# Kernel optimization log

Hardware: AMD Instinct MI355X
Metric: run time of the kernel (lower is better)

## Reference

```python
import jax, jax.numpy as jnp
import numpy as np

N_ATOMS = 100000
N_BONDS = 250000
MAX_NB = 6
HIDDEN = 256
DEPTH = 3
NUM_MOLS = 2000
ATOM_FDIM = 133
BOND_FDIM = 147


def setup_inputs() -> dict:
    key = jax.random.key(0)
    ks = jax.random.split(key, 12)
    return {
        "f_atoms": jax.random.normal(ks[0], (N_ATOMS, ATOM_FDIM), jnp.float32),
        "f_bonds": jax.random.normal(ks[1], (N_BONDS, BOND_FDIM), jnp.float32),
        "w_atoms": jax.random.uniform(ks[2], (N_ATOMS,), jnp.float32),
        "w_bonds": jax.random.uniform(ks[3], (N_BONDS,), jnp.float32),
        "W_i": jax.random.normal(ks[4], (BOND_FDIM, HIDDEN), jnp.float32) * 0.05,
        "W_h": jax.random.normal(ks[5], (HIDDEN, HIDDEN), jnp.float32) * 0.05,
        "W_o": jax.random.normal(ks[6], (ATOM_FDIM + HIDDEN, HIDDEN), jnp.float32) * 0.05,
        "b_o": jnp.zeros((HIDDEN,), jnp.float32),
        "degree_of_polym": jax.random.uniform(ks[7], (NUM_MOLS,), jnp.float32),
        "a2b": jax.random.randint(ks[8], (N_ATOMS, MAX_NB), 0, N_BONDS, jnp.int32),
        "b2a": jax.random.randint(ks[9], (N_BONDS,), 0, N_ATOMS, jnp.int32),
        "b2revb": jax.random.randint(ks[10], (N_BONDS,), 0, N_BONDS, jnp.int32),
        "mol_ids": jnp.sort(jax.random.randint(ks[11], (N_ATOMS,), 0, NUM_MOLS, jnp.int32)),
    }


def reference(f_atoms, f_bonds, w_atoms, w_bonds, W_i, W_h, W_o, b_o,
              degree_of_polym, a2b, b2a, b2revb, mol_ids):
    # input-layer: bond features -> hidden messages
    inp = f_bonds @ W_i                      # [n_bonds, H]
    message = jax.nn.relu(inp)

    for _ in range(DEPTH - 1):
        # gather incoming bond messages per atom and weight them
        nei_msg = message[a2b]               # [n_atoms, max_nb, H]
        nei_w = w_bonds[a2b]                 # [n_atoms, max_nb]
        a_message = (nei_msg * nei_w[..., None]).sum(axis=1)  # [n_atoms, H]
        # directed message: total at source atom minus reverse bond
        message = a_message[b2a] - message[b2revb]             # [n_bonds, H]
        message = jax.nn.relu(inp + message @ W_h)             # dropout p=0 (eval)

    # final atom-level readout
    nei_msg = message[a2b] * w_bonds[a2b][..., None]
    a_message = nei_msg.sum(axis=1)                            # [n_atoms, H]
    a_input = jnp.concatenate([f_atoms, a_message], axis=1)    # [n_atoms, atom_fdim+H]
    atom_hiddens = jax.nn.relu(a_input @ W_o + b_o)            # [n_atoms, H]

    # per-molecule weighted mean aggregation (a_scope loop -> segment_sum)
    weighted = atom_hiddens * w_atoms[:, None]
    mol_sum = jax.ops.segment_sum(weighted, mol_ids, num_segments=NUM_MOLS)
    w_sum = jax.ops.segment_sum(w_atoms, mol_ids, num_segments=NUM_MOLS)
    safe_w = jnp.where(w_sum > 0, w_sum, 1.0)
    mol_vecs = jnp.where((w_sum > 0)[:, None], mol_sum / safe_w[:, None], 0.0)
    mol_vecs = degree_of_polym[:, None] * mol_vecs             # [num_mols, H]
    return mol_vecs
```

## Files before the change

### kernel.cpp

```cpp
#include <hip/hip_runtime.h>
#include <hip/hip_bf16.h>

typedef unsigned short u16;
typedef __bf16 bf16x8v __attribute__((ext_vector_type(8)));
typedef float f32x4v __attribute__((ext_vector_type(4)));
typedef float f32x4u __attribute__((ext_vector_type(4))) __attribute__((aligned(4)));

__device__ __forceinline__ float bf2f(u16 u) {
    union { float f; unsigned int i; } c; c.i = ((unsigned int)u) << 16; return c.f;
}
__device__ __forceinline__ u16 f2bf(float f) {
    union { float f; unsigned int i; } c; c.f = f;
    unsigned int i = c.i;
    unsigned int lsb = (i >> 16) & 1u;
    i += 0x7fffu + lsb;
    return (u16)(i >> 16);
}
__device__ __forceinline__ float lo16(unsigned u) { return bf2f((u16)(u & 0xffff)); }
__device__ __forceinline__ float hi16(unsigned u) { return bf2f((u16)(u >> 16)); }
__device__ __forceinline__ unsigned pack2(float lo, float hi) {
    return (unsigned)f2bf(lo) | ((unsigned)f2bf(hi) << 16);
}

__device__ __forceinline__ unsigned neg2(unsigned u) { return u ^ 0x80008000u; }
__device__ __forceinline__ unsigned relu_neg2(unsigned u) {
    unsigned s = u & 0x80008000u;
    unsigned m = (s - (s >> 15)) | s;
    return (u ^ 0x80008000u) & ~m;
}

__device__ __forceinline__ bf16x8v load_cvt8(const float* __restrict__ rowp, int k, int kmax) {
    union { unsigned u[4]; bf16x8v v; } r;
#pragma unroll
    for (int g = 0; g < 2; ++g) {
        int kk = k + g * 4;
        float f0, f1, f2, f3;
        if (kk + 3 < kmax) {
            f32x4u q = *(const f32x4u*)(rowp + kk);
            f0 = q.x; f1 = q.y; f2 = q.z; f3 = q.w;
        } else {
            f0 = (kk + 0 < kmax) ? rowp[kk + 0] : 0.f;
            f1 = (kk + 1 < kmax) ? rowp[kk + 1] : 0.f;
            f2 = (kk + 2 < kmax) ? rowp[kk + 2] : 0.f;
            f3 = (kk + 3 < kmax) ? rowp[kk + 3] : 0.f;
        }
        r.u[g * 2]     = pack2(f0, f1);
        r.u[g * 2 + 1] = pack2(f2, f3);
    }
    return r.v;
}

__global__ void pack_w(const float* __restrict__ W, u16* __restrict__ Wt, int K, int Kpad) {
    int idx = blockIdx.x * 256 + threadIdx.x;
    if (idx >= 256 * Kpad) return;
    int n = idx / Kpad, k = idx % Kpad;
    float v = (k < K) ? W[k * 256 + n] : 0.f;
    Wt[idx] = f2bf(v);
}

__global__ void pack_wo(const float* __restrict__ W_o, u16* __restrict__ Wt) {
    int idx = blockIdx.x * 256 + threadIdx.x;
    if (idx >= 256 * 448) return;
    int n = idx / 448, k = idx % 448;
    float v;
    if (k < 256)       v = W_o[(133 + k) * 256 + n];
    else if (k < 389)  v = W_o[(k - 256) * 256 + n];
    else               v = 0.f;
    Wt[idx] = f2bf(v);
}

template <bool RELU>
__global__ __launch_bounds__(256)
void gather16(const u16* __restrict__ msg, const int* __restrict__ a2b,
              const float* __restrict__ w_bonds, u16* __restrict__ out, int nAtoms) {
    int t = threadIdx.x;
    int atom = blockIdx.x * 8 + (t >> 5);
    int co = (t & 31) * 8;
    if (atom >= nAtoms) return;
    float a[8] = {0.f, 0.f, 0.f, 0.f, 0.f, 0.f, 0.f, 0.f};
#pragma unroll
    for (int j = 0; j < 6; ++j) {
        int b = a2b[atom * 6 + j];
        float w = w_bonds[b];
        uint4 v = *(const uint4*)(msg + (size_t)b * 256 + co);
        unsigned p[4] = {v.x, v.y, v.z, v.w};
#pragma unroll
        for (int q = 0; q < 4; ++q) {
            float m0 = lo16(p[q]), m1 = hi16(p[q]);
            if (RELU) { m0 = fmaxf(m0, 0.f); m1 = fmaxf(m1, 0.f); }
            a[q * 2]     += w * m0;
            a[q * 2 + 1] += w * m1;
        }
    }
    uint4 o;
    o.x = pack2(a[0], a[1]); o.y = pack2(a[2], a[3]);
    o.z = pack2(a[4], a[5]); o.w = pack2(a[6], a[7]);
    *(uint4*)(out + (size_t)atom * 256 + co) = o;
}

__global__ __launch_bounds__(512, 2)
void gemm_in(const float* __restrict__ A, const u16* __restrict__ Bt, int M,
             u16* __restrict__ out0) {
    constexpr int KPAD = 160, KMAX = 147, ASTR = 147;
    constexpr int LSTR = KPAD + 8;
    __shared__ u16 Bs[256 * LSTR];
    const int tid = threadIdx.x;
    const int wave = tid >> 6;
    const int lane = tid & 63;
    const int mrow = lane & 15;
    const int quad = lane >> 4;

    constexpr int KC = KPAD / 8;
    for (int i = tid; i < 256 * KC; i += 512) {
        int r = i / KC, kc = i % KC;
        *(uint4*)&Bs[r * LSTR + kc * 8] = *(const uint4*)&Bt[(size_t)r * KPAD + kc * 8];
    }
    __syncthreads();

    for (long chunk = blockIdx.x; chunk * 256 < (long)M; chunk += gridDim.x) {
        const long mbase = chunk * 256 + wave * 32;
        const float* rowp[2];
#pragma unroll
        for (int t = 0; t < 2; ++t) {
            long r = mbase + t * 16 + mrow;
            if (r >= M) r = M - 1;
            rowp[t] = A + r * ASTR;
        }

        f32x4v acc[2][16];
#pragma unroll
        for (int t = 0; t < 2; ++t)
#pragma unroll
            for (int j = 0; j < 16; ++j) acc[t][j] = (f32x4v){0.f, 0.f, 0.f, 0.f};

#pragma unroll 2
        for (int k0 = 0; k0 < KPAD; k0 += 32) {
            bf16x8v a_frag[2];
#pragma unroll
            for (int t = 0; t < 2; ++t)
                a_frag[t] = load_cvt8(rowp[t], k0 + quad * 8, KMAX);
#pragma unroll
            for (int jg = 0; jg < 4; ++jg) {
                bf16x8v b_frag[4];
#pragma unroll
                for (int j4 = 0; j4 < 4; ++j4)
                    b_frag[j4] = *(const bf16x8v*)&Bs[((jg * 4 + j4) * 16 + mrow) * LSTR + k0 + quad * 8];
#pragma unroll
                for (int t = 0; t < 2; ++t)
#pragma unroll
                    for (int j4 = 0; j4 < 4; ++j4)
                        acc[t][jg * 4 + j4] = __builtin_amdgcn_mfma_f32_16x16x32_bf16(
                            a_frag[t], b_frag[j4], acc[t][jg * 4 + j4], 0, 0, 0);
            }
        }

#pragma unroll
        for (int t = 0; t < 2; ++t)
#pragma unroll
            for (int r = 0; r < 4; ++r) {
                long grow = mbase + t * 16 + quad * 4 + r;
                if (grow < M)
#pragma unroll
                    for (int j = 0; j < 16; ++j)
                        out0[(size_t)grow * 256 + j * 16 + mrow] = f2bf(acc[t][j][r]);
            }
    }
}

template <bool RELUV>
__global__ __launch_bounds__(512, 4)
void gemm_mp(const u16* __restrict__ amsg, const u16* __restrict__ msgsrc,
             const int* __restrict__ b2a, const int* __restrict__ b2revb,
             const u16* __restrict__ Bt, int M,
             const u16* __restrict__ inp, u16* __restrict__ out0) {
    constexpr int KPAD = 256;
    constexpr int LSTR = KPAD + 8;
    constexpr int NROWS = 128;
    __shared__ u16 Bs[NROWS * LSTR];
    const int tid = threadIdx.x;
    const int wave = tid >> 6;
    const int lane = tid & 63;
    const int mrow = lane & 15;
    const int quad = lane >> 4;

    const int nch = (M + 255) >> 8;
    const int cpx = (nch + 7) >> 3;
    const int bid = blockIdx.x;
    const int xcd = bid & 7;
    const int seq = bid >> 3;
    const long chunk = (long)xcd * cpx + (seq >> 1);
    if (chunk >= nch) return;
    const int nbase = (seq & 1) * NROWS;

    constexpr int KC = KPAD / 8;
    for (int i = tid; i < NROWS * KC; i += 512) {
        int r = i / KC, kc = i % KC;
        *(uint4*)&Bs[r * LSTR + kc * 8] = *(const uint4*)&Bt[(size_t)(nbase + r) * KPAD + kc * 8];
    }
    __syncthreads();

    const long mbase = chunk * 256 + wave * 32;
    size_t soff[2], roff[2];
#pragma unroll
    for (int t = 0; t < 2; ++t) {
        long b = mbase + t * 16 + mrow;
        if (b >= M) b = M - 1;
        soff[t] = (size_t)b2a[b] * 256 + quad * 8;
        roff[t] = (size_t)b2revb[b] * 256 + quad * 8;
    }

    f32x4v acc[2][8];
#pragma unroll
    for (int t = 0; t < 2; ++t)
#pragma unroll
        for (int j = 0; j < 8; ++j) acc[t][j] = (f32x4v){0.f, 0.f, 0.f, 0.f};

#pragma unroll 2
    for (int k0 = 0; k0 < KPAD; k0 += 32) {
        bf16x8v a1[2], a2[2];
#pragma unroll
        for (int t = 0; t < 2; ++t) {
            union { uint4 q; bf16x8v v; } ua, ur;
            ua.q = *(const uint4*)&amsg[soff[t] + k0];
            uint4 vr = *(const uint4*)&msgsrc[roff[t] + k0];
            if (RELUV) {
                ur.q.x = relu_neg2(vr.x); ur.q.y = relu_neg2(vr.y);
                ur.q.z = relu_neg2(vr.z); ur.q.w = relu_neg2(vr.w);
            } else {
                ur.q.x = neg2(vr.x); ur.q.y = neg2(vr.y);
                ur.q.z = neg2(vr.z); ur.q.w = neg2(vr.w);
            }
            a1[t] = ua.v;
            a2[t] = ur.v;
        }
#pragma unroll
        for (int jg = 0; jg < 2; ++jg) {
            bf16x8v b_frag[4];
#pragma unroll
            for (int j4 = 0; j4 < 4; ++j4)
                b_frag[j4] = *(const bf16x8v*)&Bs[((jg * 4 + j4) * 16 + mrow) * LSTR + k0 + quad * 8];
#pragma unroll
            for (int t = 0; t < 2; ++t)
#pragma unroll
                for (int j4 = 0; j4 < 4; ++j4) {
                    acc[t][jg * 4 + j4] = __builtin_amdgcn_mfma_f32_16x16x32_bf16(
                        a1[t], b_frag[j4], acc[t][jg * 4 + j4], 0, 0, 0);
                    acc[t][jg * 4 + j4] = __builtin_amdgcn_mfma_f32_16x16x32_bf16(
                        a2[t], b_frag[j4], acc[t][jg * 4 + j4], 0, 0, 0);
                }
        }
    }

#pragma unroll
    for (int t = 0; t < 2; ++t)
#pragma unroll
        for (int r = 0; r < 4; ++r) {
            long grow = mbase + t * 16 + quad * 4 + r;
            if (grow < M)
#pragma unroll
                for (int j = 0; j < 8; ++j) {
                    size_t idx = (size_t)grow * 256 + nbase + j * 16 + mrow;
                    float s = bf2f(inp[idx]) + acc[t][j][r];
                    out0[idx] = f2bf(s > 0.f ? s : 0.f);
                }
        }
}

__global__ __launch_bounds__(512, 2)
void gemm_ro(const u16* __restrict__ A1, const float* __restrict__ A2,
             const u16* __restrict__ Bt, int M,
             const float* __restrict__ bias, float* __restrict__ outf) {
    constexpr int KPAD = 448, KSPLIT = 256, K2 = 192, KMAX2 = 133;
    constexpr int LSTR = KPAD + 8;
    constexpr int NROWS = 128;
    __shared__ u16 Bs[NROWS * LSTR];
    const int tid = threadIdx.x;
    const int wave = tid >> 6;
    const int lane = tid & 63;
    const int mrow = lane & 15;
    const int quad = lane >> 4;

    const int nch = (M + 255) >> 8;
    const int cpx = (nch + 7) >> 3;
    const int bid = blockIdx.x;
    const int xcd = bid & 7;
    const int seq = bid >> 3;
    const long chunk = (long)xcd * cpx + (seq >> 1);
    if (chunk >= nch) return;
    const int nbase = (seq & 1) * NROWS;

    constexpr int KC = KPAD / 8;
    for (int i = tid; i < NROWS * KC; i += 512) {
        int r = i / KC, kc = i % KC;
        *(uint4*)&Bs[r * LSTR + kc * 8] =
            *(const uint4*)&Bt[(size_t)(nbase + r) * KPAD + kc * 8];
    }
    __syncthreads();

    const long mbase = chunk * 256 + wave * 32;
    long row[2];
#pragma unroll
    for (int t = 0; t < 2; ++t) {
        long r = mbase + t * 16 + mrow;
        if (r >= M) r = M - 1;
        row[t] = r;
    }

    f32x4v acc[2][8];
#pragma unroll
    for (int t = 0; t < 2; ++t)
#pragma unroll
        for (int j = 0; j < 8; ++j) acc[t][j] = (f32x4v){0.f, 0.f, 0.f, 0.f};

#pragma unroll 2
    for (int k0 = 0; k0 < KSPLIT; k0 += 32) {
        bf16x8v a_frag[2], b_frag[8];
#pragma unroll
        for (int t = 0; t < 2; ++t)
            a_frag[t] = *(const bf16x8v*)&A1[row[t] * KSPLIT + k0 + quad * 8];
#pragma unroll
        for (int j = 0; j < 8; ++j)
            b_frag[j] = *(const bf16x8v*)&Bs[(j * 16 + mrow) * LSTR + k0 + quad * 8];
#pragma unroll
        for (int t = 0; t < 2; ++t)
#pragma unroll
            for (int j = 0; j < 8; ++j)
                acc[t][j] = __builtin_amdgcn_mfma_f32_16x16x32_bf16(
                    a_frag[t], b_frag[j], acc[t][j], 0, 0, 0);
    }
#pragma unroll 2
    for (int k0 = 0; k0 < K2; k0 += 32) {
        bf16x8v a_frag[2], b_frag[8];
#pragma unroll
        for (int t = 0; t < 2; ++t)
            a_frag[t] = load_cvt8(A2 + row[t] * KMAX2, k0 + quad * 8, KMAX2);
#pragma unroll
        for (int j = 0; j < 8; ++j)
            b_frag[j] = *(const bf16x8v*)&Bs[(j * 16 + mrow) * LSTR + KSPLIT + k0 + quad * 8];
#pragma unroll
        for (int t = 0; t < 2; ++t)
#pragma unroll
            for (int j = 0; j < 8; ++j)
                acc[t][j] = __builtin_amdgcn_mfma_f32_16x16x32_bf16(
                    a_frag[t], b_frag[j], acc[t][j], 0, 0, 0);
    }

#pragma unroll
    for (int t = 0; t < 2; ++t)
#pragma unroll
        for (int r = 0; r < 4; ++r) {
            long grow = mbase + t * 16 + quad * 4 + r;
            if (grow < M)
#pragma unroll
                for (int j = 0; j < 8; ++j) {
                    int gcol = nbase + j * 16 + mrow;
                    float s = acc[t][j][r] + bias[gcol];
                    outf[(size_t)grow * 256 + gcol] = s > 0.f ? s : 0.f;
                }
        }
}

__global__ __launch_bounds__(256)
void aggregate_kernel(const float* __restrict__ hid, const float* __restrict__ w_atoms,
                      const int* __restrict__ mol_ids, const float* __restrict__ deg,
                      float* __restrict__ out, int nAtoms) {
    int m = blockIdx.x;
    int t = threadIdx.x;
    int lo = 0, hi = nAtoms;
    while (lo < hi) { int mid = (lo + hi) >> 1; if (mol_ids[mid] < m) lo = mid + 1; else hi = mid; }
    int start = lo;
    lo = start; hi = nAtoms;
    while (lo < hi) { int mid = (lo + hi) >> 1; if (mol_ids[mid] < m + 1) lo = mid + 1; else hi = mid; }
    int end = lo;
    float acc = 0.f, wsum = 0.f;
    for (int a = start; a < end; ++a) {
        float w = w_atoms[a];
        wsum += w;
        acc += w * hid[(size_t)a * 256 + t];
    }
    float res = (wsum > 0.f) ? deg[m] * acc / wsum : 0.f;
    out[m * 256 + t] = res;
}

extern "C" void kernel_launch(void* const* d_in, const int* in_sizes, int n_in,
                              void* d_out, int out_size, void* d_ws, size_t ws_size,
                              hipStream_t stream) {
    const float* f_atoms = (const float*)d_in[0];
    const float* f_bonds = (const float*)d_in[1];
    const float* w_atoms = (const float*)d_in[2];
    const float* w_bonds = (const float*)d_in[3];
    const float* W_i     = (const float*)d_in[4];
    const float* W_h     = (const float*)d_in[5];
    const float* W_o     = (const float*)d_in[6];
    const float* b_o     = (const float*)d_in[7];
    const float* deg     = (const float*)d_in[8];
    const int*   a2b     = (const int*)d_in[9];
    const int*   b2a     = (const int*)d_in[10];
    const int*   b2revb  = (const int*)d_in[11];
    const int*   mol_ids = (const int*)d_in[12];
    float* out = (float*)d_out;

    const int nB = 250000, nA = 100000, nM = 2000;

    char* ws = (char*)d_ws;
    u16* inp    = (u16*)(ws);
    u16* msgA   = (u16*)(ws + 128000000L);
    float* hid  = (float*)(ws + 256000000L);
    u16* amsg   = (u16*)(ws + 384000000L);
    u16* wt_i   = (u16*)(ws + 435200000L);
    u16* wt_h   = (u16*)(ws + 435200000L + 81920L);
    u16* wt_o   = (u16*)(ws + 435200000L + 81920L + 131072L);

    if (ws_size < 435642368UL) return;

    dim3 b256(256), b512(512);
    pack_w<<<dim3((256 * 160 + 255) / 256), b256, 0, stream>>>(W_i, wt_i, 147, 160);
    pack_w<<<dim3((256 * 256 + 255) / 256), b256, 0, stream>>>(W_h, wt_h, 256, 256);
    pack_wo<<<dim3((256 * 448 + 255) / 256), b256, 0, stream>>>(W_o, wt_o);

    gemm_in<<<dim3(977), b512, 0, stream>>>(f_bonds, wt_i, nB, inp);

    const int nchB = (nB + 255) >> 8, cpxB = (nchB + 7) >> 3;
    dim3 gmp(8 * cpxB * 2);
    const int nchA = (nA + 255) >> 8, cpxA = (nchA + 7) >> 3;
    dim3 gro(8 * cpxA * 2);

    gather16<true><<<dim3(nA / 8), b256, 0, stream>>>(inp, a2b, w_bonds, amsg, nA);
    gemm_mp<true><<<gmp, b512, 0, stream>>>(
        amsg, inp, b2a, b2revb, wt_h, nB, inp, msgA);

    gather16<false><<<dim3(nA / 8), b256, 0, stream>>>(msgA, a2b, w_bonds, amsg, nA);
    gemm_mp<false><<<gmp, b512, 0, stream>>>(
        amsg, msgA, b2a, b2revb, wt_h, nB, inp, inp);

    gather16<false><<<dim3(nA / 8), b256, 0, stream>>>(inp , a2b, w_bonds, amsg, nA);
    gemm_ro<<<gro, b512, 0, stream>>>(amsg, f_atoms, wt_o, nA, b_o, hid);

    aggregate_kernel<<<dim3(nM), b256, 0, stream>>>(hid, w_atoms, mol_ids, deg, out, nA);
}
```

Measured before the change: 863.4 us.

## Fuse neighbor gather-sum into message-passing and readout GEMM kernels

Removes the standalone per-atom gather kernels and instead computes the weighted neighbor sum on the fly inside gemm_mp (per bond via its source atom) and gemm_ro (per atom). This eliminates the intermediate atom-message buffer write/read and three kernel launches. In exchange, gemm_mp redoes the 6-way gather for every bond rather than once per atom, which increases random global loads, and its tile is halved to 16 rows per wave.

```diff
diff --git a/kernel.cpp b/kernel.cpp
--- a/kernel.cpp
+++ b/kernel.cpp
@@ -23,6 +23,11 @@
 }
 
 __device__ __forceinline__ unsigned neg2(unsigned u) { return u ^ 0x80008000u; }
+__device__ __forceinline__ unsigned relu2(unsigned u) {
+    unsigned s = u & 0x80008000u;
+    unsigned m = (s - (s >> 15)) | s;
+    return u & ~m;
+}
 __device__ __forceinline__ unsigned relu_neg2(unsigned u) {
     unsigned s = u & 0x80008000u;
     unsigned m = (s - (s >> 15)) | s;
@@ -69,35 +74,6 @@
     Wt[idx] = f2bf(v);
 }
 
-template <bool RELU>
-__global__ __launch_bounds__(256)
-void gather16(const u16* __restrict__ msg, const int* __restrict__ a2b,
-              const float* __restrict__ w_bonds, u16* __restrict__ out, int nAtoms) {
-    int t = threadIdx.x;
-    int atom = blockIdx.x * 8 + (t >> 5);
-    int co = (t & 31) * 8;
-    if (atom >= nAtoms) return;
-    float a[8] = {0.f, 0.f, 0.f, 0.f, 0.f, 0.f, 0.f, 0.f};
-#pragma unroll
-    for (int j = 0; j < 6; ++j) {
-        int b = a2b[atom * 6 + j];
-        float w = w_bonds[b];
-        uint4 v = *(const uint4*)(msg + (size_t)b * 256 + co);
-        unsigned p[4] = {v.x, v.y, v.z, v.w};
-#pragma unroll
-        for (int q = 0; q < 4; ++q) {
-            float m0 = lo16(p[q]), m1 = hi16(p[q]);
-            if (RELU) { m0 = fmaxf(m0, 0.f); m1 = fmaxf(m1, 0.f); }
-            a[q * 2]     += w * m0;
-            a[q * 2 + 1] += w * m1;
-        }
-    }
-    uint4 o;
-    o.x = pack2(a[0], a[1]); o.y = pack2(a[2], a[3]);
-    o.z = pack2(a[4], a[5]); o.w = pack2(a[6], a[7]);
-    *(uint4*)(out + (size_t)atom * 256 + co) = o;
-}
-
 __global__ __launch_bounds__(512, 2)
 void gemm_in(const float* __restrict__ A, const u16* __restrict__ Bt, int M,
              u16* __restrict__ out0) {
@@ -169,10 +145,10 @@
 
 template <bool RELUV>
 __global__ __launch_bounds__(512, 4)
-void gemm_mp(const u16* __restrict__ amsg, const u16* __restrict__ msgsrc,
+void gemm_mp(const u16* __restrict__ msg, const int* __restrict__ a2b,
              const int* __restrict__ b2a, const int* __restrict__ b2revb,
-             const u16* __restrict__ Bt, int M,
-             const u16* __restrict__ inp, u16* __restrict__ out0) {
+             const float* __restrict__ w_bonds, const u16* __restrict__ Bt,
+             int M, const u16* __restrict__ inp, u16* __restrict__ out0) {
     constexpr int KPAD = 256;
     constexpr int LSTR = KPAD + 8;
     constexpr int NROWS = 128;
@@ -183,6 +159,108 @@
     const int mrow = lane & 15;
     const int quad = lane >> 4;
 
+    const int nch = (M + 127) >> 7;
+    const int cpx = (nch + 7) >> 3;
+    const int bid = blockIdx.x;
+    const int xcd = bid & 7;
+    const int seq = bid >> 3;
+    const long chunk = (long)xcd * cpx + (seq >> 1);
+    if (chunk >= nch) return;
+    const int nbase = (seq & 1) * NROWS;
+
+    constexpr int KC = KPAD / 8;
+    for (int i = tid; i < NROWS * KC; i += 512) {
+        int r = i / KC, kc = i % KC;
+        *(uint4*)&Bs[r * LSTR + kc * 8] = *(const uint4*)&Bt[(size_t)(nbase + r) * KPAD + kc * 8];
+    }
+    __syncthreads();
+
+    const long mbase = chunk * 128 + wave * 16;
+    long b = mbase + mrow;
+    if (b >= M) b = M - 1;
+    const int sa = b2a[b];
+    unsigned joff[6];
+    float jw[6];
+#pragma unroll
+    for (int j = 0; j < 6; ++j) {
+        int r = a2b[sa * 6 + j];
+        joff[j] = (unsigned)r * 512u + quad * 16u;
+        jw[j] = w_bonds[r];
+    }
+    const unsigned roff = (unsigned)b2revb[b] * 512u + quad * 16u;
+    const char* msgB = (const char*)msg;
+
+    f32x4v acc[8];
+#pragma unroll
+    for (int j = 0; j < 8; ++j) acc[j] = (f32x4v){0.f, 0.f, 0.f, 0.f};
+
+#pragma unroll 2
+    for (int ke = 0; ke < KPAD; ke += 32) {
+        const int kb = ke * 2;
+        uint4 vj[6];
+#pragma unroll
+        for (int j = 0; j < 6; ++j)
+            vj[j] = *(const uint4*)(msgB + joff[j] + kb);
+        uint4 vr = *(const uint4*)(msgB + roff + kb);
+
+        float s[8] = {0.f, 0.f, 0.f, 0.f, 0.f, 0.f, 0.f, 0.f};
+#pragma unroll
+        for (int j = 0; j < 6; ++j) {
+            unsigned p0 = vj[j].x, p1 = vj[j].y, p2 = vj[j].z, p3 = vj[j].w;
+            if (RELUV) { p0 = relu2(p0); p1 = relu2(p1); p2 = relu2(p2); p3 = relu2(p3); }
+            const float w = jw[j];
+            s[0] += w * lo16(p0); s[1] += w * hi16(p0);
+            s[2] += w * lo16(p1); s[3] += w * hi16(p1);
+            s[4] += w * lo16(p2); s[5] += w * hi16(p2);
+            s[6] += w * lo16(p3); s[7] += w * hi16(p3);
+        }
+        union { unsigned u[4]; bf16x8v v; } ua, ur;
+        ua.u[0] = pack2(s[0], s[1]); ua.u[1] = pack2(s[2], s[3]);
+        ua.u[2] = pack2(s[4], s[5]); ua.u[3] = pack2(s[6], s[7]);
+        if (RELUV) {
+            ur.u[0] = relu_neg2(vr.x); ur.u[1] = relu_neg2(vr.y);
+            ur.u[2] = relu_neg2(vr.z); ur.u[3] = relu_neg2(vr.w);
+        } else {
+            ur.u[0] = neg2(vr.x); ur.u[1] = neg2(vr.y);
+            ur.u[2] = neg2(vr.z); ur.u[3] = neg2(vr.w);
+        }
+
+#pragma unroll
+        for (int j8 = 0; j8 < 8; ++j8) {
+            bf16x8v b_frag = *(const bf16x8v*)&Bs[(j8 * 16 + mrow) * LSTR + ke + quad * 8];
+            acc[j8] = __builtin_amdgcn_mfma_f32_16x16x32_bf16(ua.v, b_frag, acc[j8], 0, 0, 0);
+            acc[j8] = __builtin_amdgcn_mfma_f32_16x16x32_bf16(ur.v, b_frag, acc[j8], 0, 0, 0);
+        }
+    }
+
+#pragma unroll
+    for (int r = 0; r < 4; ++r) {
+        long grow = mbase + quad * 4 + r;
+        if (grow < M)
+#pragma unroll
+            for (int j8 = 0; j8 < 8; ++j8) {
+                size_t idx = (size_t)grow * 256 + nbase + j8 * 16 + mrow;
+                float s = bf2f(inp[idx]) + acc[j8][r];
+                out0[idx] = f2bf(s > 0.f ? s : 0.f);
+            }
+    }
+}
+
+__global__ __launch_bounds__(512, 2)
+void gemm_ro(const u16* __restrict__ msgT, const int* __restrict__ a2b,
+             const float* __restrict__ w_bonds, const float* __restrict__ A2,
+             const u16* __restrict__ Bt, int M,
+             const float* __restrict__ bias, float* __restrict__ outf) {
+    constexpr int KSPLIT = 256, K2 = 192, KMAX2 = 133, KPAD = 448;
+    constexpr int LSTR = KPAD + 8;
+    constexpr int NROWS = 128;
+    __shared__ u16 Bs[NROWS * LSTR];
+    const int tid = threadIdx.x;
+    const int wave = tid >> 6;
+    const int lane = tid & 63;
+    const int mrow = lane & 15;
+    const int quad = lane >> 4;
+
     const int nch = (M + 255) >> 8;
     const int cpx = (nch + 7) >> 3;
     const int bid = blockIdx.x;
@@ -195,103 +273,6 @@
     constexpr int KC = KPAD / 8;
     for (int i = tid; i < NROWS * KC; i += 512) {
         int r = i / KC, kc = i % KC;
-        *(uint4*)&Bs[r * LSTR + kc * 8] = *(const uint4*)&Bt[(size_t)(nbase + r) * KPAD + kc * 8];
-    }
-    __syncthreads();
-
-    const long mbase = chunk * 256 + wave * 32;
-    size_t soff[2], roff[2];
-#pragma unroll
-    for (int t = 0; t < 2; ++t) {
-        long b = mbase + t * 16 + mrow;
-        if (b >= M) b = M - 1;
-        soff[t] = (size_t)b2a[b] * 256 + quad * 8;
-        roff[t] = (size_t)b2revb[b] * 256 + quad * 8;
-    }
-
-    f32x4v acc[2][8];
-#pragma unroll
-    for (int t = 0; t < 2; ++t)
-#pragma unroll
-        for (int j = 0; j < 8; ++j) acc[t][j] = (f32x4v){0.f, 0.f, 0.f, 0.f};
-
-#pragma unroll 2
-    for (int k0 = 0; k0 < KPAD; k0 += 32) {
-        bf16x8v a1[2], a2[2];
-#pragma unroll
-        for (int t = 0; t < 2; ++t) {
-            union { uint4 q; bf16x8v v; } ua, ur;
-            ua.q = *(const uint4*)&amsg[soff[t] + k0];
-            uint4 vr = *(const uint4*)&msgsrc[roff[t] + k0];
-            if (RELUV) {
-                ur.q.x = relu_neg2(vr.x); ur.q.y = relu_neg2(vr.y);
-                ur.q.z = relu_neg2(vr.z); ur.q.w = relu_neg2(vr.w);
-            } else {
-                ur.q.x = neg2(vr.x); ur.q.y = neg2(vr.y);
-                ur.q.z = neg2(vr.z); ur.q.w = neg2(vr.w);
-            }
-            a1[t] = ua.v;
-            a2[t] = ur.v;
-        }
-#pragma unroll
-        for (int jg = 0; jg < 2; ++jg) {
-            bf16x8v b_frag[4];
-#pragma unroll
-            for (int j4 = 0; j4 < 4; ++j4)
-                b_frag[j4] = *(const bf16x8v*)&Bs[((jg * 4 + j4) * 16 + mrow) * LSTR + k0 + quad * 8];
-#pragma unroll
-            for (int t = 0; t < 2; ++t)
-#pragma unroll
-                for (int j4 = 0; j4 < 4; ++j4) {
-                    acc[t][jg * 4 + j4] = __builtin_amdgcn_mfma_f32_16x16x32_bf16(
-                        a1[t], b_frag[j4], acc[t][jg * 4 + j4], 0, 0, 0);
-                    acc[t][jg * 4 + j4] = __builtin_amdgcn_mfma_f32_16x16x32_bf16(
-                        a2[t], b_frag[j4], acc[t][jg * 4 + j4], 0, 0, 0);
-                }
-        }
-    }
-
-#pragma unroll
-    for (int t = 0; t < 2; ++t)
-#pragma unroll
-        for (int r = 0; r < 4; ++r) {
-            long grow = mbase + t * 16 + quad * 4 + r;
-            if (grow < M)
-#pragma unroll
-                for (int j = 0; j < 8; ++j) {
-                    size_t idx = (size_t)grow * 256 + nbase + j * 16 + mrow;
-                    float s = bf2f(inp[idx]) + acc[t][j][r];
-                    out0[idx] = f2bf(s > 0.f ? s : 0.f);
-                }
-        }
-}
-
-__global__ __launch_bounds__(512, 2)
-void gemm_ro(const u16* __restrict__ A1, const float* __restrict__ A2,
-             const u16* __restrict__ Bt, int M,
-             const float* __restrict__ bias, float* __restrict__ outf) {
-    constexpr int KPAD = 448, KSPLIT = 256, K2 = 192, KMAX2 = 133;
-    constexpr int LSTR = KPAD + 8;
-    constexpr int NROWS = 128;
-    __shared__ u16 Bs[NROWS * LSTR];
-    const int tid = threadIdx.x;
-    const int wave = tid >> 6;
-    const int lane = tid & 63;
-    const int mrow = lane & 15;
-    const int quad = lane >> 4;
-
-    const int nch = (M + 255) >> 8;
-    const int cpx = (nch + 7) >> 3;
-    const int bid = blockIdx.x;
-    const int xcd = bid & 7;
-    const int seq = bid >> 3;
-    const long chunk = (long)xcd * cpx + (seq >> 1);
-    if (chunk >= nch) return;
-    const int nbase = (seq & 1) * NROWS;
-
-    constexpr int KC = KPAD / 8;
-    for (int i = tid; i < NROWS * KC; i += 512) {
-        int r = i / KC, kc = i % KC;
         *(uint4*)&Bs[r * LSTR + kc * 8] =
             *(const uint4*)&Bt[(size_t)(nbase + r) * KPAD + kc * 8];
     }
@@ -299,12 +280,21 @@
 
     const long mbase = chunk * 256 + wave * 32;
     long row[2];
+    unsigned joff[2][6];
+    float jw[2][6];
 #pragma unroll
     for (int t = 0; t < 2; ++t) {
         long r = mbase + t * 16 + mrow;
         if (r >= M) r = M - 1;
         row[t] = r;
-    }
+#pragma unroll
+        for (int j = 0; j < 6; ++j) {
+            int br = a2b[r * 6 + j];
+            joff[t][j] = (unsigned)br * 512u + quad * 16u;
+            jw[t][j] = w_bonds[br];
+        }
+    }
+    const char* msgB = (const char*)msgT;
 
     f32x4v acc[2][8];
 #pragma unroll
@@ -313,20 +303,37 @@
         for (int j = 0; j < 8; ++j) acc[t][j] = (f32x4v){0.f, 0.f, 0.f, 0.f};
 
 #pragma unroll 2
-    for (int k0 = 0; k0 < KSPLIT; k0 += 32) {
-        bf16x8v a_frag[2], b_frag[8];
-#pragma unroll
-        for (int t = 0; t < 2; ++t)
-            a_frag[t] = *(const bf16x8v*)&A1[row[t] * KSPLIT + k0 + quad * 8];
-#pragma unroll
-        for (int j = 0; j < 8; ++j)
-            b_frag[j] = *(const bf16x8v*)&Bs[(j * 16 + mrow) * LSTR + k0 + quad * 8];
-#pragma unroll
-        for (int t = 0; t < 2; ++t)
-#pragma unroll
-            for (int j = 0; j < 8; ++j)
+    for (int ke = 0; ke < KSPLIT; ke += 32) {
+        const int kb = ke * 2;
+        bf16x8v a_frag[2];
+#pragma unroll
+        for (int t = 0; t < 2; ++t) {
+            uint4 vj[6];
+#pragma unroll
+            for (int j = 0; j < 6; ++j)
+                vj[j] = *(const uint4*)(msgB + joff[t][j] + kb);
+            float s[8] = {0.f, 0.f, 0.f, 0.f, 0.f, 0.f, 0.f, 0.f};
+#pragma unroll
+            for (int j = 0; j < 6; ++j) {
+                const float w = jw[t][j];
+                s[0] += w * lo16(vj[j].x); s[1] += w * hi16(vj[j].x);
+                s[2] += w * lo16(vj[j].y); s[3] += w * hi16(vj[j].y);
+                s[4] += w * lo16(vj[j].z); s[5] += w * hi16(vj[j].z);
+                s[6] += w * lo16(vj[j].w); s[7] += w * hi16(vj[j].w);
+            }
+            union { unsigned u[4]; bf16x8v v; } ua;
+            ua.u[0] = pack2(s[0], s[1]); ua.u[1] = pack2(s[2], s[3]);
+            ua.u[2] = pack2(s[4], s[5]); ua.u[3] = pack2(s[6], s[7]);
+            a_frag[t] = ua.v;
+        }
+#pragma unroll
+        for (int j = 0; j < 8; ++j) {
+            bf16x8v b_frag = *(const bf16x8v*)&Bs[(j * 16 + mrow) * LSTR + ke + quad * 8];
+#pragma unroll
+            for (int t = 0; t < 2; ++t)
                 acc[t][j] = __builtin_amdgcn_mfma_f32_16x16x32_bf16(
-                    a_frag[t], b_frag[j], acc[t][j], 0, 0, 0);
+                    a_frag[t], b_frag, acc[t][j], 0, 0, 0);
+        }
     }
 #pragma unroll 2
     for (int k0 = 0; k0 < K2; k0 += 32) {
@@ -406,7 +413,6 @@
     u16* inp    = (u16*)(ws);
     u16* msgA   = (u16*)(ws + 128000000L);
     float* hid  = (float*)(ws + 256000000L);
-    u16* amsg   = (u16*)(ws + 384000000L);
     u16* wt_i   = (u16*)(ws + 435200000L);
     u16* wt_h   = (u16*)(ws + 435200000L + 81920L);
     u16* wt_o   = (u16*)(ws + 435200000L + 81920L + 131072L);
@@ -420,21 +426,18 @@
 
     gemm_in<<<dim3(977), b512, 0, stream>>>(f_bonds, wt_i, nB, inp);
 
-    const int nchB = (nB + 255) >> 8, cpxB = (nchB + 7) >> 3;
+    const int nchB = (nB + 127) >> 7, cpxB = (nchB + 7) >> 3;
     dim3 gmp(8 * cpxB * 2);
     const int nchA = (nA + 255) >> 8, cpxA = (nchA + 7) >> 3;
     dim3 gro(8 * cpxA * 2);
 
-    gather16<true><<<dim3(nA / 8), b256, 0, stream>>>(inp, a2b, w_bonds, amsg, nA);
     gemm_mp<true><<<gmp, b512, 0, stream>>>(
-        amsg, inp, b2a, b2revb, wt_h, nB, inp, msgA);
-
-    gather16<false><<<dim3(nA / 8), b256, 0, stream>>>(msgA, a2b, w_bonds, amsg, nA);
+        inp, a2b, b2a, b2revb, w_bonds, wt_h, nB, inp, msgA);
+
     gemm_mp<false><<<gmp, b512, 0, stream>>>(
-        amsg, msgA, b2a, b2revb, wt_h, nB, inp, inp);
-
-    gather16<false><<<dim3(nA / 8), b256, 0, stream>>>(inp , a2b, w_bonds, amsg, nA);
-    gemm_ro<<<gro, b512, 0, stream>>>(amsg, f_atoms, wt_o, nA, b_o, hid);
+        msgA, a2b, b2a, b2revb, w_bonds, wt_h, nB, inp, inp);
+
+    gemm_ro<<<gro, b512, 0, stream>>>(inp , a2b, w_bonds, f_atoms, wt_o, nA, b_o, hid);
 
     aggregate_kernel<<<dim3(nM), b256, 0, stream>>>(hid, w_atoms, mol_ids, deg, out, nA);
 }
```

Result: slower. 1.101 ms (+27.6%).
